# Kernel tuning notes

Measured on AMD Instinct MI355X. Metric: run time of the kernel, lower is better.

The kernel has to match this reference:

```python
import jax, jax.numpy as jnp
import numpy as np
from jax import lax

B, N, F_IN, T = 1024, 22, 32, 32
K = 3
CHEV = 64     # nb_chev_filter
TIMEF = 64    # nb_time_filter
LN_EPS = 1e-5


def setup_inputs() -> dict:
    key = jax.random.key(0)
    ks = jax.random.split(key, 19)
    rn = lambda k, shape, s=0.1: (jax.random.normal(k, shape, jnp.float32) * s)
    return {
        "x": rn(ks[0], (B, N, F_IN, T), 1.0),
        # Temporal_Attention_layer params
        "U1": rn(ks[1], (N,)),
        "U2": rn(ks[2], (F_IN, N)),
        "U3": rn(ks[3], (F_IN,)),
        "be": rn(ks[4], (1, T, T)),
        "Ve": rn(ks[5], (T, T)),
        # Spatial_Attention_layer params
        "W1": rn(ks[6], (T,)),
        "W2": rn(ks[7], (F_IN, T)),
        "W3": rn(ks[8], (F_IN,)),
        "bs": rn(ks[9], (1, N, N)),
        "Vs": rn(ks[10], (N, N)),
        # cheb_conv_withSAt params
        "Theta": rn(ks[11], (K, F_IN, CHEV)),
        "node_emb": rn(ks[12], (N, N), 1.0),
        # time conv (1x3, pad (0,1)) and residual conv (1x1)
        "tconv_w": rn(ks[13], (TIMEF, CHEV, 1, 3)),
        "tconv_b": rn(ks[14], (TIMEF,)),
        "rconv_w": rn(ks[15], (TIMEF, F_IN, 1, 1)),
        "rconv_b": rn(ks[16], (TIMEF,)),
        # LayerNorm over nb_time_filter
        "ln_g": jnp.ones((TIMEF,), jnp.float32),
        "ln_b": jnp.zeros((TIMEF,), jnp.float32),
    }


def reference(x, U1, U2, U3, be, Ve, W1, W2, W3, bs, Vs, Theta, node_emb,
              tconv_w, tconv_b, rconv_w, rconv_b, ln_g, ln_b):
    Bx, Nx, Fx, Tx = x.shape

    # ---- Temporal attention: E_normalized [B, T, T] ----
    # lhs = ((x.permute(0,3,2,1) @ U1) @ U2)  -> [B, T, N]
    lhs_t = jnp.einsum('bnft,n->btf', x, U1) @ U2          # [B,T,N]
    rhs_t = jnp.einsum('f,bnft->bnt', U3, x)               # [B,N,T]
    prod_t = jnp.einsum('btn,bns->bts', lhs_t, rhs_t)      # [B,T,T]
    E = jnp.einsum('ts,bsu->btu', Ve, jax.nn.sigmoid(prod_t + be))
    E_norm = jax.nn.softmax(E, axis=1)                     # softmax over dim=1

    # x_TAt = reshape(x, [B, N*F, T]) @ E_norm  -> [B, N, F, T]
    x_TAt = (x.reshape(Bx, Nx * Fx, Tx) @ E_norm).reshape(Bx, Nx, Fx, Tx)

    # ---- Spatial attention on x_TAt: S_normalized [B, N, N] ----
    lhs_s = jnp.einsum('bnft,t->bnf', x_TAt, W1) @ W2      # [B,N,T]
    rhs_s = jnp.einsum('f,bnft->bnt', W3, x_TAt)           # [B,N,T]
    prod_s = jnp.einsum('bnt,bmt->bnm', lhs_s, rhs_s)      # [B,N,N]
    S = jnp.einsum('nm,bml->bnl', Vs, jax.nn.sigmoid(prod_s + bs))
    S_norm = jax.nn.softmax(S, axis=1)                     # softmax over dim=1

    # ---- Chebyshev graph conv with adaptive supports (vectorized over T) ----
    supports = jax.nn.softmax(jax.nn.relu(node_emb @ node_emb.T), axis=1)
    support_set = [jnp.eye(Nx, dtype=x.dtype), supports]
    for _ in range(2, K):
        support_set.append(2.0 * supports @ support_set[-1] - support_set[-2])

    out = jnp.zeros((Bx, Nx, CHEV, Tx), x.dtype)
    for k in range(K):
        A_k = support_set[k][None, :, :] * S_norm          # [B,N,N]
        # rhs[b,m,f,t] = sum_n A_k[b,n,m] * x[b,n,f,t]  (A_k^T @ graph_signal)
        rhs = jnp.einsum('bnm,bnft->bmft', A_k, x)
        out = out + jnp.einsum('bmft,fo->bmot', rhs, Theta[k])
    spatial_gcn = jax.nn.relu(out)                         # [B,N,CHEV,T]

    # ---- Temporal conv (1x3, pad (0,1)) on [B, CHEV, N, T] ----
    dn = ('NCHW', 'OIHW', 'NCHW')
    t_in = spatial_gcn.transpose(0, 2, 1, 3)               # [B,CHEV,N,T]
    t_out = lax.conv_general_dilated(t_in, tconv_w, (1, 1), ((0, 0), (1, 1)),
                                     dimension_numbers=dn)
    t_out = t_out + tconv_b[None, :, None, None]           # [B,TIMEF,N,T]

    # ---- Residual conv (1x1) on [B, F_in, N, T] ----
    r_in = x.transpose(0, 2, 1, 3)
    r_out = lax.conv_general_dilated(r_in, rconv_w, (1, 1), ((0, 0), (0, 0)),
                                     dimension_numbers=dn)
    r_out = r_out + rconv_b[None, :, None, None]           # [B,TIMEF,N,T]

    # ---- Residual add, ReLU, LayerNorm over channel dim ----
    y = jax.nn.relu(r_out + t_out).transpose(0, 3, 2, 1)   # [B,T,N,TIMEF]
    mu = jnp.mean(y, axis=-1, keepdims=True)
    var = jnp.var(y, axis=-1, keepdims=True)
    y = (y - mu) * lax.rsqrt(var + LN_EPS) * ln_g + ln_b
    return y.transpose(0, 2, 3, 1)                         # [B,N,TIMEF,T]
```

## Files before the change

kernel.cpp:

```cpp
#include <hip/hip_runtime.h>
#include <hip/hip_bf16.h>
#include <math.h>


typedef unsigned short u16;
typedef __attribute__((ext_vector_type(8))) short short8;
typedef __attribute__((ext_vector_type(4))) float f32x4;
typedef __attribute__((ext_vector_type(2))) float f32x2;

__device__ __forceinline__ float sigm(float v){ return 1.f/(1.f+expf(-v)); }

__device__ __forceinline__ u16 f2bf(float x){
  __hip_bfloat16 h = __float2bfloat16(x);
  return *reinterpret_cast<u16*>(&h);
}
__device__ __forceinline__ unsigned f2bf2(float lo, float hi){
  return (unsigned)f2bf(lo) | ((unsigned)f2bf(hi) << 16);
}

__global__ void k_sup_prep(const float* __restrict__ emb, float* __restrict__ wsT,
                           const float* __restrict__ Theta,
                           const float* __restrict__ tw, const float* __restrict__ tb,
                           const float* __restrict__ rw, const float* __restrict__ rb,
                           u16* __restrict__ thA, u16* __restrict__ wA, float* __restrict__ wsB){
  if (blockIdx.x < 81){
    int tid = blockIdx.x*256 + threadIdx.x;
    if (tid < 6144){
      int j = tid&7, l = (tid>>3)&63, blk = tid>>9;
      int ks = blk>>2, ci = blk&3, r = l&15, g = l>>4;
      int kf = 32*ks + 8*g + j, c = 16*ci + r;
      thA[tid] = f2bf(Theta[kf*64 + c]);
    } else if (tid < 20480){
      int e = tid - 6144;
      int j = e&7, l = (e>>3)&63, blk = e>>9;
      int ks = blk>>2, oi = blk&3, r = l&15, g = l>>4;
      int k = 32*ks + 8*g + j, o = 16*oi + r;
      float v = (k < 192) ? tw[o*192 + (k&63)*3 + (k>>6)] : rw[o*32 + (k-192)];
      wA[e] = f2bf(v);
    } else if (tid < 20544){
      int o = tid - 20480; wsB[o] = tb[o] + rb[o];
    }
    return;
  }
  __shared__ float M[484];
  __shared__ float T1s[484];
  int tid = threadIdx.x;
  for (int idx=tid; idx<484; idx+=256){
    int n = idx/22, m = idx - (idx/22)*22;
    float s = 0.f;
    for (int j=0;j<22;j++) s += emb[n*22+j]*emb[m*22+j];
    M[idx] = fmaxf(s, 0.f);
  }
  __syncthreads();
  if (tid < 22){
    float mx = -1e30f;
    for (int m=0;m<22;m++) mx = fmaxf(mx, M[tid*22+m]);
    float s = 0.f;
    for (int m=0;m<22;m++) s += expf(M[tid*22+m]-mx);
    float inv = 1.f/s;
    for (int m=0;m<22;m++) T1s[tid*22+m] = expf(M[tid*22+m]-mx)*inv;
  }
  __syncthreads();
  for (int idx=tid; idx<484; idx+=256){
    int n = idx/22, m = idx - (idx/22)*22;
    float s = 0.f;
    for (int p=0;p<22;p++) s += T1s[n*22+p]*T1s[p*22+m];
    wsT[idx]      = T1s[idx];
    wsT[484+idx]  = 2.f*s - ((n==m)?1.f:0.f);
  }
}

__global__ __launch_bounds__(512) void k_attn(
    const float* __restrict__ x,
    const float* __restrict__ U1, const float* __restrict__ U2, const float* __restrict__ U3,
    const float* __restrict__ be, const float* __restrict__ Ve,
    const float* __restrict__ W1, const float* __restrict__ W2, const float* __restrict__ W3,
    const float* __restrict__ bs, const float* __restrict__ Vs,
    float* __restrict__ snorm){
  int b = blockIdx.x, tid = threadIdx.x;
  const float* xb = x + (size_t)b*22528;
  __shared__ float xu1[1024];
  __shared__ float rhs_t[704];
  __shared__ float lhs_t[704];
  __shared__ float sigp[1024];
  __shared__ float Em[1024];
  __shared__ float sm[1024];
  __shared__ float w1e[32];
  __shared__ float xw3[704];
  __shared__ float lhsS[704];
  __shared__ float lhs2[704];
  __shared__ float rhsS[704];
  __shared__ float sig2[484];
  __shared__ float Sl[484];

  for (int idx=tid; idx<1024; idx+=512){
    float a=0.f;
    for (int n=0;n<22;n++) a = fmaf(xb[n*1024 + idx], U1[n], a);
    xu1[idx]=a;
  }
  for (int idx=tid; idx<704; idx+=512){
    int n = idx>>5, t = idx&31; float a=0.f, c=0.f;
    for (int f=0;f<32;f++){ float xv = xb[n*1024+f*32+t]; a = fmaf(U3[f],xv,a); c = fmaf(W3[f],xv,c); }
    rhs_t[idx]=a; xw3[idx]=c;
  }
  __syncthreads();
  for (int idx=tid; idx<704; idx+=512){
    int t = idx/22, n2 = idx - t*22; float a=0.f;
    for (int f=0;f<32;f++) a = fmaf(xu1[f*32+t], U2[f*22+n2], a);
    lhs_t[idx]=a;
  }
  __syncthreads();
  for (int idx=tid; idx<1024; idx+=512){
    int s = idx>>5, u = idx&31; float p=0.f;
    for (int n=0;n<22;n++) p = fmaf(lhs_t[s*22+n], rhs_t[n*32+u], p);
    sigp[idx] = sigm(p + be[idx]);
  }
  __syncthreads();
  for (int idx=tid; idx<1024; idx+=512){
    int t = idx>>5, u = idx&31; float a=0.f;
    for (int s2=0;s2<32;s2++) a = fmaf(Ve[t*32+s2], sigp[s2*32+u], a);
    Em[idx]=a;
  }
  __syncthreads();
  {
    int u = tid>>4, th = tid&15;
    float e0 = Em[(2*th)*32 + u], e1 = Em[(2*th+1)*32 + u];
    float mx = fmaxf(e0, e1);
    #pragma unroll
    for (int mask=1; mask<16; mask<<=1) mx = fmaxf(mx, __shfl_xor(mx, mask));
    float x0 = expf(e0-mx), x1 = expf(e1-mx);
    float s = x0 + x1;
    #pragma unroll
    for (int mask=1; mask<16; mask<<=1) s += __shfl_xor(s, mask);
    float inv = 1.f/s;
    sm[(2*th)*32 + u]   = x0*inv;
    sm[(2*th+1)*32 + u] = x1*inv;
  }
  __syncthreads();
  {
    int u = tid>>4, th = tid&15;
    float pw = fmaf(sm[u*32 + 2*th], W1[2*th], sm[u*32 + 2*th+1]*W1[2*th+1]);
    #pragma unroll
    for (int mask=1; mask<16; mask<<=1) pw += __shfl_xor(pw, mask);
    if (th==0) w1e[u] = pw;
  }
  __syncthreads();
  for (int idx=tid; idx<704; idx+=512){
    int n = idx>>5, f = idx&31; float a=0.f;
    for (int u=0;u<32;u++) a = fmaf(xb[n*1024+f*32+u], w1e[u], a);
    lhsS[idx]=a;
  }
  __syncthreads();
  for (int idx=tid; idx<704; idx+=512){
    int n = idx>>5, t = idx&31; float a=0.f;
    for (int f=0;f<32;f++) a = fmaf(lhsS[n*32+f], W2[f*32+t], a);
    lhs2[idx]=a;
  }
  for (int idx=tid; idx<704; idx+=512){
    int mm = idx>>5, t = idx&31; float a=0.f;
    for (int u=0;u<32;u++) a = fmaf(xw3[mm*32+u], sm[u*32+t], a);
    rhsS[idx]=a;
  }
  __syncthreads();
  for (int idx=tid; idx<484; idx+=512){
    int a_ = idx/22, l = idx - (idx/22)*22; float p=0.f;
    for (int t=0;t<32;t++) p = fmaf(lhs2[a_*32+t], rhsS[l*32+t], p);
    sig2[idx] = sigm(p + bs[idx]);
  }
  __syncthreads();
  for (int idx=tid; idx<484; idx+=512){
    int n = idx/22, l = idx - (idx/22)*22; float s=0.f;
    for (int mm=0;mm<22;mm++) s = fmaf(Vs[n*22+mm], sig2[mm*22+l], s);
    Sl[idx]=s;
  }
  __syncthreads();
  {
    int grp = tid>>5, nn = tid&31;
    for (int l = grp; l < 22; l += 16){
      float v = (nn<22) ? Sl[nn*22 + l] : -1e30f;
      float mx = v;
      #pragma unroll
      for (int mask=1; mask<32; mask<<=1) mx = fmaxf(mx, __shfl_xor(mx, mask));
      float e = (nn<22) ? expf(v-mx) : 0.f;
      float s = e;
      #pragma unroll
      for (int mask=1; mask<32; mask<<=1) s += __shfl_xor(s, mask);
      if (nn<22) snorm[(size_t)b*484 + nn*22 + l] = e*(1.f/s);
    }
  }
}

__global__ __launch_bounds__(256, 6) void k_fused(
    const float* __restrict__ x,
    const float* __restrict__ wsT, const float* __restrict__ snorm,
    const u16* __restrict__ thA, const u16* __restrict__ wA, const float* __restrict__ wsB,
    const float* __restrict__ lng, const float* __restrict__ lnb,
    float* __restrict__ out){
  __shared__ __align__(16) u16 GtU[2][32*72];
  __shared__ __align__(16) u16 sgTU[2][34*72];
  __shared__ __align__(16) u16 xTU[2][32*40];
  __shared__ __align__(16) float ak4[22*4];
  __shared__ float smm[2];

  int wg = blockIdx.x;
  int logical = (wg & 7)*1408 + (wg >> 3);
  int b = logical/11, mp = logical - b*11;
  int m0 = mp*2;
  int tid = threadIdx.x;
  const float* xb = x + (size_t)b*22528;

  if (tid < 128){
    int mi = tid>>6, r6 = tid&63;
    int row = (r6>>5) ? 33 : 0, c2 = r6&31;
    *(unsigned*)&sgTU[mi][row*72 + c2*2] = 0u;
  }
  if (tid < 88){
    int n = tid>>2, j = tid&3;
    int mi = j>>1, k1 = j&1;
    int m = m0 + mi;
    ak4[tid] = wsT[k1*484 + n*22 + m] * snorm[(size_t)b*484 + n*22 + m];
  }
  if (tid < 2) smm[tid] = snorm[(size_t)b*484 + (m0+tid)*23];
  __syncthreads();

  {
    f32x2 acc[2][2][2];
    #pragma unroll
    for (int a=0;a<2;a++)
      #pragma unroll
      for (int k1=0;k1<2;k1++){ acc[a][k1][0]=f32x2{0,0}; acc[a][k1][1]=f32x2{0,0}; }
    const float4* x4 = (const float4*)xb;
    #pragma unroll 2
    for (int n=0;n<22;n++){
      float4 av = *(const float4*)&ak4[n*4];
      float4 xv = x4[n*256 + tid];
      f32x2 xlo = {xv.x, xv.y}, xhi = {xv.z, xv.w};
      f32x2 a00 = {av.x, av.x}, a01 = {av.y, av.y};
      f32x2 a10 = {av.z, av.z}, a11 = {av.w, av.w};
      acc[0][0][0] = __builtin_elementwise_fma(a00, xlo, acc[0][0][0]);
      acc[0][0][1] = __builtin_elementwise_fma(a00, xhi, acc[0][0][1]);
      acc[0][1][0] = __builtin_elementwise_fma(a01, xlo, acc[0][1][0]);
      acc[0][1][1] = __builtin_elementwise_fma(a01, xhi, acc[0][1][1]);
      acc[1][0][0] = __builtin_elementwise_fma(a10, xlo, acc[1][0][0]);
      acc[1][0][1] = __builtin_elementwise_fma(a10, xhi, acc[1][0][1]);
      acc[1][1][0] = __builtin_elementwise_fma(a11, xlo, acc[1][1][0]);
      acc[1][1][1] = __builtin_elementwise_fma(a11, xhi, acc[1][1][1]);
    }
    int f = tid>>3, t7 = tid&7, t0 = t7*4;
    int w4 = f>>3, f_low = f&7;
    int gcol0 = 8*((0*4 + w4) ^ t7) + f_low;
    int gcol1 = 8*((1*4 + w4) ^ t7) + f_low;
    int xcol  = 8*(w4 ^ (t7&3)) + f_low;
    #pragma unroll
    for (int mi=0;mi<2;mi++){
      float4 xm = ((const float4*)xb)[(m0+mi)*256 + tid];
      u16* xd = &xTU[mi][0];
      xd[(t0+0)*40 + xcol] = f2bf(xm.x);
      xd[(t0+1)*40 + xcol] = f2bf(xm.y);
      xd[(t0+2)*40 + xcol] = f2bf(xm.z);
      xd[(t0+3)*40 + xcol] = f2bf(xm.w);
      #pragma unroll
      for (int k1=0;k1<2;k1++){
        int gc = k1 ? gcol1 : gcol0;
        u16* gd = &GtU[mi][gc];
        gd[(t0+0)*72] = f2bf(acc[mi][k1][0][0]);
        gd[(t0+1)*72] = f2bf(acc[mi][k1][0][1]);
        gd[(t0+2)*72] = f2bf(acc[mi][k1][1][0]);
        gd[(t0+3)*72] = f2bf(acc[mi][k1][1][1]);
      }
    }
  }
  __syncthreads();

  int w = tid>>6, l = tid&63, r = l&15, g = l>>4;

  {
    const u16* tA = thA + (size_t)(w*64 + l)*8;
    short8 a0 = *(const short8*)(tA);
    short8 a1 = *(const short8*)(tA + 2048);
    short8 a2 = *(const short8*)(tA + 4096);
    #pragma unroll
    for (int mi=0;mi<2;mi++){
      float sm_ = smm[mi];
      #pragma unroll
      for (int ti=0; ti<2; ++ti){
        int row = ti*16 + r;
        int h  = (row>>2)&7;
        int h2 = (row>>2)&3;
        f32x4 a12 = {0.f,0.f,0.f,0.f}, ax = {0.f,0.f,0.f,0.f};
        const u16* gp0 = &GtU[mi][row*72 + 8*((0*4+g)^h)];
        const u16* gp1 = &GtU[mi][row*72 + 8*((1*4+g)^h)];
        a12 = __builtin_amdgcn_mfma_f32_16x16x32_bf16(a1, *(const short8*)(gp0), a12, 0,0,0);
        a12 = __builtin_amdgcn_mfma_f32_16x16x32_bf16(a2, *(const short8*)(gp1), a12, 0,0,0);
        const u16* xp = &xTU[mi][row*40 + 8*(g^h2)];
        ax  = __builtin_amdgcn_mfma_f32_16x16x32_bf16(a0, *(const short8*)(xp),  ax,  0,0,0);
        int orow = 1 + row, c0 = w*16 + g*4;
        float v0 = fmaxf(fmaf(sm_, ax[0], a12[0]), 0.f);
        float v1 = fmaxf(fmaf(sm_, ax[1], a12[1]), 0.f);
        float v2 = fmaxf(fmaf(sm_, ax[2], a12[2]), 0.f);
        float v3 = fmaxf(fmaf(sm_, ax[3], a12[3]), 0.f);
        *(unsigned*)&sgTU[mi][orow*72 + c0]     = f2bf2(v0, v1);
        *(unsigned*)&sgTU[mi][orow*72 + c0 + 2] = f2bf2(v2, v3);
      }
    }
  }
  __syncthreads();

  f32x4 acc[2][2];
  acc[0][0]=f32x4{0,0,0,0}; acc[0][1]=f32x4{0,0,0,0};
  acc[1][0]=f32x4{0,0,0,0}; acc[1][1]=f32x4{0,0,0,0};
  {
    const u16* pA = wA + (size_t)(w*64 + l)*8;
    #pragma unroll
    for (int ks=0; ks<6; ++ks){
      short8 wk = *(const short8*)(pA + ks*2048);
      int seg = ks>>1, colb = (ks&1)*32 + 8*g;
      #pragma unroll
      for (int mi=0;mi<2;mi++){
        const u16* q0 = &sgTU[mi][(r + seg)*72 + colb];
        acc[mi][0] = __builtin_amdgcn_mfma_f32_16x16x32_bf16(wk, *(const short8*)(q0),         acc[mi][0], 0,0,0);
        acc[mi][1] = __builtin_amdgcn_mfma_f32_16x16x32_bf16(wk, *(const short8*)(q0 + 16*72), acc[mi][1], 0,0,0);
      }
    }
    short8 wk = *(const short8*)(pA + 6*2048);
    int h2 = (r>>2)&3;
    #pragma unroll
    for (int mi=0;mi<2;mi++){
      const u16* q = &xTU[mi][r*40 + 8*(g^h2)];
      acc[mi][0] = __builtin_amdgcn_mfma_f32_16x16x32_bf16(wk, *(const short8*)(q),         acc[mi][0], 0,0,0);
      acc[mi][1] = __builtin_amdgcn_mfma_f32_16x16x32_bf16(wk, *(const short8*)(q + 16*40), acc[mi][1], 0,0,0);
    }
  }

  float4 bias4 = ((const float4*)wsB)[w*4 + g];
  float bb[4] = {bias4.x, bias4.y, bias4.z, bias4.w};
  float y[2][2][4];
  float s1[2][2] = {{0.f,0.f},{0.f,0.f}}, s2[2][2] = {{0.f,0.f},{0.f,0.f}};
  #pragma unroll
  for (int mi=0;mi<2;mi++){
    #pragma unroll
    for (int h=0;h<2;h++){
      #pragma unroll
      for (int i=0;i<4;i++){
        float v = fmaxf(acc[mi][h][i] + bb[i], 0.f);
        y[mi][h][i] = v;
        s1[mi][h] += v;
        s2[mi][h] = fmaf(v, v, s2[mi][h]);
      }
      s1[mi][h] += __shfl_xor(s1[mi][h],16); s1[mi][h] += __shfl_xor(s1[mi][h],32);
      s2[mi][h] += __shfl_xor(s2[mi][h],16); s2[mi][h] += __shfl_xor(s2[mi][h],32);
    }
  }
  float* p1 = (float*)&GtU[0][0];
  float* p2 = p1 + 256;
  if (l < 16){
    #pragma unroll
    for (int mi=0;mi<2;mi++){
      p1[(mi*32 + l)*4 + w]      = s1[mi][0];
      p1[(mi*32 + 16 + l)*4 + w] = s1[mi][1];
      p2[(mi*32 + l)*4 + w]      = s2[mi][0];
      p2[(mi*32 + 16 + l)*4 + w] = s2[mi][1];
    }
  }
  __syncthreads();
  float4 g4 = ((const float4*)lng)[w*4 + g];
  float4 b4 = ((const float4*)lnb)[w*4 + g];
  float gg[4]={g4.x,g4.y,g4.z,g4.w}, bgg[4]={b4.x,b4.y,b4.z,b4.w};
  #pragma unroll
  for (int mi=0;mi<2;mi++){
    float4 q1a = ((const float4*)p1)[mi*32 + r],      q2a = ((const float4*)p2)[mi*32 + r];
    float4 q1b = ((const float4*)p1)[mi*32 + 16 + r], q2b = ((const float4*)p2)[mi*32 + 16 + r];
    float S1a = q1a.x+q1a.y+q1a.z+q1a.w, S2a = q2a.x+q2a.y+q2a.z+q2a.w;
    float S1b = q1b.x+q1b.y+q1b.z+q1b.w, S2b = q2b.x+q2b.y+q2b.z+q2b.w;
    float mu0 = S1a*(1.f/64.f), var0 = S2a*(1.f/64.f) - mu0*mu0, rs0 = rsqrtf(var0 + 1e-5f);
    float mu1 = S1b*(1.f/64.f), var1 = S2b*(1.f/64.f) - mu1*mu1, rs1 = rsqrtf(var1 + 1e-5f);
    float* ob = out + ((size_t)(b*22 + m0 + mi)*64 + (w*16 + g*4))*32;
    #pragma unroll
    for (int i=0;i<4;i++){
      ob[i*32 + r]      = (y[mi][0][i]-mu0)*rs0*gg[i] + bgg[i];
      ob[i*32 + 16 + r] = (y[mi][1][i]-mu1)*rs1*gg[i] + bgg[i];
    }
  }
}

extern "C" void kernel_launch(void* const* d_in, const int* in_sizes, int n_in,
                              void* d_out, int out_size, void* d_ws, size_t ws_size,
                              hipStream_t stream){
  const float* x     = (const float*)d_in[0];
  const float* U1    = (const float*)d_in[1];
  const float* U2    = (const float*)d_in[2];
  const float* U3    = (const float*)d_in[3];
  const float* be    = (const float*)d_in[4];
  const float* Ve    = (const float*)d_in[5];
  const float* W1    = (const float*)d_in[6];
  const float* W2    = (const float*)d_in[7];
  const float* W3    = (const float*)d_in[8];
  const float* bs    = (const float*)d_in[9];
  const float* Vs    = (const float*)d_in[10];
  const float* Theta = (const float*)d_in[11];
  const float* emb   = (const float*)d_in[12];
  const float* tw    = (const float*)d_in[13];
  const float* tb    = (const float*)d_in[14];
  const float* rw    = (const float*)d_in[15];
  const float* rb    = (const float*)d_in[16];
  const float* lng   = (const float*)d_in[17];
  const float* lnb   = (const float*)d_in[18];
  float* out = (float*)d_out;
  float* wsf = (float*)d_ws;
  float* wsT   = wsf;
  float* snorm = wsf + 1024;
  u16*   thA   = (u16*)(wsf + 496640);
  u16*   wA    = (u16*)(wsf + 499712);
  float* wsB   = wsf + 506880;

  k_sup_prep<<<82, 256, 0, stream>>>(emb, wsT, Theta, tw, tb, rw, rb, thA, wA, wsB);
  k_attn<<<1024, 512, 0, stream>>>(x, U1,U2,U3, be,Ve, W1,W2,W3, bs,Vs, snorm);
  k_fused<<<1024*11, 256, 0, stream>>>(x, wsT, snorm, thA, wA, wsB, lng, lnb, out);
}
```

Baseline: 152.1 us.

## Switch fused kernel MFMAs to 32x32x16 tiles with per-wave node/channel split

Replaces the 16x16x32 bf16 MFMA tiling in both the Chebyshev and temporal-conv GEMMs with 32x32x16 MFMAs. Each wave now owns one output node and one 32-channel half instead of a 16-channel slice across both nodes. Weight pre-packing in the prep kernel is reordered to match. The x gather and the LDS layout are changed to unswizzled, vectorized uint2 stores, and the LayerNorm reduction is simplified to two partial sums. Occupancy bound drops from 6 to 5 to allow the larger accumulators, at the risk of LDS bank conflicts from the removed swizzle.

After: 160.8 us. +5.8%, slower.

```diff
diff --git a/kernel.cpp b/kernel.cpp
--- a/kernel.cpp
+++ b/kernel.cpp
@@ -5,7 +5,7 @@
 
 typedef unsigned short u16;
 typedef __attribute__((ext_vector_type(8))) short short8;
-typedef __attribute__((ext_vector_type(4))) float f32x4;
+typedef __attribute__((ext_vector_type(16))) float f32x16;
 typedef __attribute__((ext_vector_type(2))) float f32x2;
 
 __device__ __forceinline__ float sigm(float v){ return 1.f/(1.f+expf(-v)); }
@@ -26,15 +26,18 @@
   if (blockIdx.x < 81){
     int tid = blockIdx.x*256 + threadIdx.x;
     if (tid < 6144){
-      int j = tid&7, l = (tid>>3)&63, blk = tid>>9;
-      int ks = blk>>2, ci = blk&3, r = l&15, g = l>>4;
-      int kf = 32*ks + 8*g + j, c = 16*ci + r;
-      thA[tid] = f2bf(Theta[kf*64 + c]);
+      int j = tid&7, l = (tid>>3)&63, slot = tid>>9;
+      int fb = slot>>1, ch = slot&1;
+      int hi = l>>5, r = l&31;
+      int row = (fb < 4) ? (32 + 16*fb + 8*hi + j) : (16*(fb-4) + 8*hi + j);
+      thA[tid] = f2bf(Theta[row*64 + 32*ch + r]);
     } else if (tid < 20480){
       int e = tid - 6144;
-      int j = e&7, l = (e>>3)&63, blk = e>>9;
-      int ks = blk>>2, oi = blk&3, r = l&15, g = l>>4;
-      int k = 32*ks + 8*g + j, o = 16*oi + r;
+      int j = e&7, l = (e>>3)&63, slot = e>>9;
+      int kb = slot>>1, oh = slot&1;
+      int hi = l>>5, r = l&31;
+      int k = 16*kb + 8*hi + j;
+      int o = 32*oh + r;
       float v = (k < 192) ? tw[o*192 + (k&63)*3 + (k>>6)] : rw[o*32 + (k-192)];
       wA[e] = f2bf(v);
     } else if (tid < 20544){
@@ -190,7 +193,7 @@
   }
 }
 
-__global__ __launch_bounds__(256, 6) void k_fused(
+__global__ __launch_bounds__(256, 5) void k_fused(
     const float* __restrict__ x,
     const float* __restrict__ wsT, const float* __restrict__ snorm,
     const u16* __restrict__ thA, const u16* __restrict__ wA, const float* __restrict__ wsB,
@@ -210,9 +213,9 @@
   const float* xb = x + (size_t)b*22528;
 
   if (tid < 128){
-    int mi = tid>>6, r6 = tid&63;
-    int row = (r6>>5) ? 33 : 0, c2 = r6&31;
-    *(unsigned*)&sgTU[mi][row*72 + c2*2] = 0u;
+    int mi = tid>>6, c = tid&63;
+    sgTU[mi][c] = 0;
+    sgTU[mi][33*72 + c] = 0;
   }
   if (tid < 88){
     int n = tid>>2, j = tid&3;
@@ -223,162 +226,146 @@
   if (tid < 2) smm[tid] = snorm[(size_t)b*484 + (m0+tid)*23];
   __syncthreads();
 
-  {
-    f32x2 acc[2][2][2];
-    #pragma unroll
-    for (int a=0;a<2;a++)
-      #pragma unroll
-      for (int k1=0;k1<2;k1++){ acc[a][k1][0]=f32x2{0,0}; acc[a][k1][1]=f32x2{0,0}; }
-    const float4* x4 = (const float4*)xb;
+  int t32 = tid&31;
+
+  {
+    int fq = tid>>5, f0 = fq*4;
+    const float* xt = xb + f0*32 + t32;
+    f32x2 acc[4][2];
+    #pragma unroll
+    for (int j=0;j<4;j++){ acc[j][0]=f32x2{0,0}; acc[j][1]=f32x2{0,0}; }
     #pragma unroll 2
     for (int n=0;n<22;n++){
       float4 av = *(const float4*)&ak4[n*4];
-      float4 xv = x4[n*256 + tid];
-      f32x2 xlo = {xv.x, xv.y}, xhi = {xv.z, xv.w};
-      f32x2 a00 = {av.x, av.x}, a01 = {av.y, av.y};
-      f32x2 a10 = {av.z, av.z}, a11 = {av.w, av.w};
-      acc[0][0][0] = __builtin_elementwise_fma(a00, xlo, acc[0][0][0]);
-      acc[0][0][1] = __builtin_elementwise_fma(a00, xhi, acc[0][0][1]);
-      acc[0][1][0] = __builtin_elementwise_fma(a01, xlo, acc[0][1][0]);
-      acc[0][1][1] = __builtin_elementwise_fma(a01, xhi, acc[0][1][1]);
-      acc[1][0][0] = __builtin_elementwise_fma(a10, xlo, acc[1][0][0]);
-      acc[1][0][1] = __builtin_elementwise_fma(a10, xhi, acc[1][0][1]);
-      acc[1][1][0] = __builtin_elementwise_fma(a11, xlo, acc[1][1][0]);
-      acc[1][1][1] = __builtin_elementwise_fma(a11, xhi, acc[1][1][1]);
-    }
-    int f = tid>>3, t7 = tid&7, t0 = t7*4;
-    int w4 = f>>3, f_low = f&7;
-    int gcol0 = 8*((0*4 + w4) ^ t7) + f_low;
-    int gcol1 = 8*((1*4 + w4) ^ t7) + f_low;
-    int xcol  = 8*(w4 ^ (t7&3)) + f_low;
+      const float* p = xt + n*1024;
+      float x0 = p[0], x1 = p[32], x2 = p[64], x3 = p[96];
+      f32x2 lo = {x0,x1}, hi2 = {x2,x3};
+      f32x2 c0 = {av.x,av.x}, c1 = {av.y,av.y}, c2 = {av.z,av.z}, c3 = {av.w,av.w};
+      acc[0][0] = __builtin_elementwise_fma(c0, lo,  acc[0][0]);
+      acc[0][1] = __builtin_elementwise_fma(c0, hi2, acc[0][1]);
+      acc[1][0] = __builtin_elementwise_fma(c1, lo,  acc[1][0]);
+      acc[1][1] = __builtin_elementwise_fma(c1, hi2, acc[1][1]);
+      acc[2][0] = __builtin_elementwise_fma(c2, lo,  acc[2][0]);
+      acc[2][1] = __builtin_elementwise_fma(c2, hi2, acc[2][1]);
+      acc[3][0] = __builtin_elementwise_fma(c3, lo,  acc[3][0]);
+      acc[3][1] = __builtin_elementwise_fma(c3, hi2, acc[3][1]);
+    }
     #pragma unroll
     for (int mi=0;mi<2;mi++){
-      float4 xm = ((const float4*)xb)[(m0+mi)*256 + tid];
-      u16* xd = &xTU[mi][0];
-      xd[(t0+0)*40 + xcol] = f2bf(xm.x);
-      xd[(t0+1)*40 + xcol] = f2bf(xm.y);
-      xd[(t0+2)*40 + xcol] = f2bf(xm.z);
-      xd[(t0+3)*40 + xcol] = f2bf(xm.w);
       #pragma unroll
       for (int k1=0;k1<2;k1++){
-        int gc = k1 ? gcol1 : gcol0;
-        u16* gd = &GtU[mi][gc];
-        gd[(t0+0)*72] = f2bf(acc[mi][k1][0][0]);
-        gd[(t0+1)*72] = f2bf(acc[mi][k1][0][1]);
-        gd[(t0+2)*72] = f2bf(acc[mi][k1][1][0]);
-        gd[(t0+3)*72] = f2bf(acc[mi][k1][1][1]);
+        int j = mi*2 + k1;
+        uint2 v; v.x = f2bf2(acc[j][0][0], acc[j][0][1]); v.y = f2bf2(acc[j][1][0], acc[j][1][1]);
+        *(uint2*)&GtU[mi][t32*72 + k1*32 + f0] = v;
       }
-    }
-  }
-  __syncthreads();
-
-  int w = tid>>6, l = tid&63, r = l&15, g = l>>4;
-
-  {
-    const u16* tA = thA + (size_t)(w*64 + l)*8;
-    short8 a0 = *(const short8*)(tA);
-    short8 a1 = *(const short8*)(tA + 2048);
-    short8 a2 = *(const short8*)(tA + 4096);
-    #pragma unroll
-    for (int mi=0;mi<2;mi++){
-      float sm_ = smm[mi];
+      const float* q = xb + (m0+mi)*1024 + f0*32 + t32;
+      float y0 = q[0], y1 = q[32], y2 = q[64], y3 = q[96];
+      uint2 v; v.x = f2bf2(y0,y1); v.y = f2bf2(y2,y3);
+      *(uint2*)&xTU[mi][t32*40 + f0] = v;
+    }
+  }
+  __syncthreads();
+
+  int w = tid>>6, l = tid&63, hi = l>>5;
+  int mi = w>>1, ch = w&1;
+  int lt = l&31;
+
+  {
+    f32x16 aG, aX;
+    #pragma unroll
+    for (int i=0;i<16;i++){ aG[i]=0.f; aX[i]=0.f; }
+    const u16* gRow = &GtU[mi][lt*72 + 8*hi];
+    const u16* xRow = &xTU[mi][lt*40 + 8*hi];
+    #pragma unroll
+    for (int fb=0; fb<4; ++fb){
+      short8 a = *(const short8*)(thA + (size_t)(fb*2+ch)*512 + l*8);
+      aG = __builtin_amdgcn_mfma_f32_32x32x16_bf16(a, *(const short8*)(gRow + 16*fb), aG, 0,0,0);
+    }
+    #pragma unroll
+    for (int fb=4; fb<6; ++fb){
+      short8 a = *(const short8*)(thA + (size_t)(fb*2+ch)*512 + l*8);
+      aX = __builtin_amdgcn_mfma_f32_32x32x16_bf16(a, *(const short8*)(xRow + 16*(fb-4)), aX, 0,0,0);
+    }
+    float smv = smm[mi];
+    u16* srow = &sgTU[mi][(1+lt)*72 + ch*32 + 4*hi];
+    #pragma unroll
+    for (int q=0;q<4;q++){
+      float v0 = fmaxf(fmaf(smv, aX[4*q+0], aG[4*q+0]), 0.f);
+      float v1 = fmaxf(fmaf(smv, aX[4*q+1], aG[4*q+1]), 0.f);
+      float v2 = fmaxf(fmaf(smv, aX[4*q+2], aG[4*q+2]), 0.f);
+      float v3 = fmaxf(fmaf(smv, aX[4*q+3], aG[4*q+3]), 0.f);
+      uint2 pv; pv.x = f2bf2(v0,v1); pv.y = f2bf2(v2,v3);
+      *(uint2*)&srow[8*q] = pv;
+    }
+  }
+  __syncthreads();
+
+  f32x16 acc;
+  #pragma unroll
+  for (int i=0;i<16;i++) acc[i]=0.f;
+  {
+    #pragma unroll
+    for (int kb=0; kb<12; ++kb){
+      int dt = kb>>2, cq = kb&3;
+      short8 wk = *(const short8*)(wA + (size_t)(kb*2+ch)*512 + l*8);
+      const short8* Bp = (const short8*)&sgTU[mi][(lt+dt)*72 + cq*16 + 8*hi];
+      acc = __builtin_amdgcn_mfma_f32_32x32x16_bf16(wk, *Bp, acc, 0,0,0);
+    }
+    #pragma unroll
+    for (int kb=12; kb<14; ++kb){
+      short8 wk = *(const short8*)(wA + (size_t)(kb*2+ch)*512 + l*8);
+      const short8* Bp = (const short8*)&xTU[mi][lt*40 + (kb-12)*16 + 8*hi];
+      acc = __builtin_amdgcn_mfma_f32_32x32x16_bf16(wk, *Bp, acc, 0,0,0);
+    }
+  }
+
+  float y[16];
+  float s1 = 0.f, s2 = 0.f;
+  {
+    const float4* wsB4 = (const float4*)wsB;
+    #pragma unroll
+    for (int q=0;q<4;q++){
+      float4 bq = wsB4[8*ch + 2*q + hi];
+      float bb[4] = {bq.x, bq.y, bq.z, bq.w};
       #pragma unroll
-      for (int ti=0; ti<2; ++ti){
-        int row = ti*16 + r;
-        int h  = (row>>2)&7;
-        int h2 = (row>>2)&3;
-        f32x4 a12 = {0.f,0.f,0.f,0.f}, ax = {0.f,0.f,0.f,0.f};
-        const u16* gp0 = &GtU[mi][row*72 + 8*((0*4+g)^h)];
-        const u16* gp1 = &GtU[mi][row*72 + 8*((1*4+g)^h)];
-        a12 = __builtin_amdgcn_mfma_f32_16x16x32_bf16(a1, *(const short8*)(gp0), a12, 0,0,0);
-        a12 = __builtin_amdgcn_mfma_f32_16x16x32_bf16(a2, *(const short8*)(gp1), a12, 0,0,0);
-        const u16* xp = &xTU[mi][row*40 + 8*(g^h2)];
-        ax  = __builtin_amdgcn_mfma_f32_16x16x32_bf16(a0, *(const short8*)(xp),  ax,  0,0,0);
-        int orow = 1 + row, c0 = w*16 + g*4;
-        float v0 = fmaxf(fmaf(sm_, ax[0], a12[0]), 0.f);
-        float v1 = fmaxf(fmaf(sm_, ax[1], a12[1]), 0.f);
-        float v2 = fmaxf(fmaf(sm_, ax[2], a12[2]), 0.f);
-        float v3 = fmaxf(fmaf(sm_, ax[3], a12[3]), 0.f);
-        *(unsigned*)&sgTU[mi][orow*72 + c0]     = f2bf2(v0, v1);
-        *(unsigned*)&sgTU[mi][orow*72 + c0 + 2] = f2bf2(v2, v3);
+      for (int e=0;e<4;e++){
+        float v = fmaxf(acc[4*q+e] + bb[e], 0.f);
+        y[4*q+e] = v;
+        s1 += v;
+        s2 = fmaf(v, v, s2);
       }
     }
   }
-  __syncthreads();
-
-  f32x4 acc[2][2];
-  acc[0][0]=f32x4{0,0,0,0}; acc[0][1]=f32x4{0,0,0,0};
-  acc[1][0]=f32x4{0,0,0,0}; acc[1][1]=f32x4{0,0,0,0};
-  {
-    const u16* pA = wA + (size_t)(w*64 + l)*8;
-    #pragma unroll
-    for (int ks=0; ks<6; ++ks){
-      short8 wk = *(const short8*)(pA + ks*2048);
-      int seg = ks>>1, colb = (ks&1)*32 + 8*g;
+  s1 += __shfl_xor(s1, 32);
+  s2 += __shfl_xor(s2, 32);
+  float* p1 = (float*)&GtU[0][0];
+  float* p2 = p1 + 128;
+  if (l < 32){
+    p1[(mi*32 + lt)*2 + ch] = s1;
+    p2[(mi*32 + lt)*2 + ch] = s2;
+  }
+  __syncthreads();
+  f32x2 q1 = *(const f32x2*)&p1[(mi*32 + lt)*2];
+  f32x2 q2 = *(const f32x2*)&p2[(mi*32 + lt)*2];
+  float S1 = q1[0] + q1[1], S2 = q2[0] + q2[1];
+  float mu = S1*(1.f/64.f);
+  float var = S2*(1.f/64.f) - mu*mu;
+  float rs = rsqrtf(var + 1e-5f);
+  {
+    const float4* lng4 = (const float4*)lng;
+    const float4* lnb4 = (const float4*)lnb;
+    float* ob = out + ((size_t)(b*22 + m0 + mi)*64 + 32*ch)*32;
+    #pragma unroll
+    for (int q=0;q<4;q++){
+      float4 g4 = lng4[8*ch + 2*q + hi];
+      float4 b4 = lnb4[8*ch + 2*q + hi];
+      float gg[4] = {g4.x,g4.y,g4.z,g4.w};
+      float bg[4] = {b4.x,b4.y,b4.z,b4.w};
       #pragma unroll
-      for (int mi=0;mi<2;mi++){
-        const u16* q0 = &sgTU[mi][(r + seg)*72 + colb];
-        acc[mi][0] = __builtin_amdgcn_mfma_f32_16x16x32_bf16(wk, *(const short8*)(q0),         acc[mi][0], 0,0,0);
-        acc[mi][1] = __builtin_amdgcn_mfma_f32_16x16x32_bf16(wk, *(const short8*)(q0 + 16*72), acc[mi][1], 0,0,0);
+      for (int e=0;e<4;e++){
+        int orow = 8*q + 4*hi + e;
+        ob[orow*32 + lt] = (y[4*q+e]-mu)*rs*gg[e] + bg[e];
       }
-    }
-    short8 wk = *(const short8*)(pA + 6*2048);
-    int h2 = (r>>2)&3;
-    #pragma unroll
-    for (int mi=0;mi<2;mi++){
-      const u16* q = &xTU[mi][r*40 + 8*(g^h2)];
-      acc[mi][0] = __builtin_amdgcn_mfma_f32_16x16x32_bf16(wk, *(const short8*)(q),         acc[mi][0], 0,0,0);
-      acc[mi][1] = __builtin_amdgcn_mfma_f32_16x16x32_bf16(wk, *(const short8*)(q + 16*40), acc[mi][1], 0,0,0);
-    }
-  }
-
-  float4 bias4 = ((const float4*)wsB)[w*4 + g];
-  float bb[4] = {bias4.x, bias4.y, bias4.z, bias4.w};
-  float y[2][2][4];
-  float s1[2][2] = {{0.f,0.f},{0.f,0.f}}, s2[2][2] = {{0.f,0.f},{0.f,0.f}};
-  #pragma unroll
-  for (int mi=0;mi<2;mi++){
-    #pragma unroll
-    for (int h=0;h<2;h++){
-      #pragma unroll
-      for (int i=0;i<4;i++){
-        float v = fmaxf(acc[mi][h][i] + bb[i], 0.f);
-        y[mi][h][i] = v;
-        s1[mi][h] += v;
-        s2[mi][h] = fmaf(v, v, s2[mi][h]);
-      }
-      s1[mi][h] += __shfl_xor(s1[mi][h],16); s1[mi][h] += __shfl_xor(s1[mi][h],32);
-      s2[mi][h] += __shfl_xor(s2[mi][h],16); s2[mi][h] += __shfl_xor(s2[mi][h],32);
-    }
-  }
-  float* p1 = (float*)&GtU[0][0];
-  float* p2 = p1 + 256;
-  if (l < 16){
-    #pragma unroll
-    for (int mi=0;mi<2;mi++){
-      p1[(mi*32 + l)*4 + w]      = s1[mi][0];
-      p1[(mi*32 + 16 + l)*4 + w] = s1[mi][1];
-      p2[(mi*32 + l)*4 + w]      = s2[mi][0];
-      p2[(mi*32 + 16 + l)*4 + w] = s2[mi][1];
-    }
-  }
-  __syncthreads();
-  float4 g4 = ((const float4*)lng)[w*4 + g];
-  float4 b4 = ((const float4*)lnb)[w*4 + g];
-  float gg[4]={g4.x,g4.y,g4.z,g4.w}, bgg[4]={b4.x,b4.y,b4.z,b4.w};
-  #pragma unroll
-  for (int mi=0;mi<2;mi++){
-    float4 q1a = ((const float4*)p1)[mi*32 + r],      q2a = ((const float4*)p2)[mi*32 + r];
-    float4 q1b = ((const float4*)p1)[mi*32 + 16 + r], q2b = ((const float4*)p2)[mi*32 + 16 + r];
-    float S1a = q1a.x+q1a.y+q1a.z+q1a.w, S2a = q2a.x+q2a.y+q2a.z+q2a.w;
-    float S1b = q1b.x+q1b.y+q1b.z+q1b.w, S2b = q2b.x+q2b.y+q2b.z+q2b.w;
-    float mu0 = S1a*(1.f/64.f), var0 = S2a*(1.f/64.f) - mu0*mu0, rs0 = rsqrtf(var0 + 1e-5f);
-    float mu1 = S1b*(1.f/64.f), var1 = S2b*(1.f/64.f) - mu1*mu1, rs1 = rsqrtf(var1 + 1e-5f);
-    float* ob = out + ((size_t)(b*22 + m0 + mi)*64 + (w*16 + g*4))*32;
-    #pragma unroll
-    for (int i=0;i<4;i++){
-      ob[i*32 + r]      = (y[mi][0][i]-mu0)*rs0*gg[i] + bgg[i];
-      ob[i*32 + 16 + r] = (y[mi][1][i]-mu1)*rs1*gg[i] + bgg[i];
     }
   }
 }
```

## Split attention kernel in two and fold weight prep into the first

Applied to the files above, without the earlier changes.

Splits the monolithic attention kernel into two kernels. The first computes the temporal-attention softmax, w1e and xw3 and writes them to global workspace. The second reloads them and computes spatial attention, so each kernel holds less shared memory and can run more blocks per CU. The separate setup kernel (weight packing, Chebyshev supports) is merged into extra blocks of the first kernel to save a launch. The lhsS dot product is vectorised with float4 loads. The cost is an extra global round trip of roughly 7 MB of intermediates plus another kernel boundary.

Result: no change. 153.9 us (+1.2%).

```diff
diff --git a/kernel.cpp b/kernel.cpp
--- a/kernel.cpp
+++ b/kernel.cpp
@@ -18,136 +18,170 @@
   return (unsigned)f2bf(lo) | ((unsigned)f2bf(hi) << 16);
 }
 
-__global__ void k_sup_prep(const float* __restrict__ emb, float* __restrict__ wsT,
-                           const float* __restrict__ Theta,
-                           const float* __restrict__ tw, const float* __restrict__ tb,
-                           const float* __restrict__ rw, const float* __restrict__ rb,
-                           u16* __restrict__ thA, u16* __restrict__ wA, float* __restrict__ wsB){
-  if (blockIdx.x < 81){
-    int tid = blockIdx.x*256 + threadIdx.x;
-    if (tid < 6144){
-      int j = tid&7, l = (tid>>3)&63, blk = tid>>9;
-      int ks = blk>>2, ci = blk&3, r = l&15, g = l>>4;
-      int kf = 32*ks + 8*g + j, c = 16*ci + r;
-      thA[tid] = f2bf(Theta[kf*64 + c]);
-    } else if (tid < 20480){
-      int e = tid - 6144;
-      int j = e&7, l = (e>>3)&63, blk = e>>9;
-      int ks = blk>>2, oi = blk&3, r = l&15, g = l>>4;
-      int k = 32*ks + 8*g + j, o = 16*oi + r;
-      float v = (k < 192) ? tw[o*192 + (k&63)*3 + (k>>6)] : rw[o*32 + (k-192)];
-      wA[e] = f2bf(v);
-    } else if (tid < 20544){
-      int o = tid - 20480; wsB[o] = tb[o] + rb[o];
-    }
-    return;
-  }
-  __shared__ float M[484];
-  __shared__ float T1s[484];
-  int tid = threadIdx.x;
-  for (int idx=tid; idx<484; idx+=256){
-    int n = idx/22, m = idx - (idx/22)*22;
-    float s = 0.f;
-    for (int j=0;j<22;j++) s += emb[n*22+j]*emb[m*22+j];
-    M[idx] = fmaxf(s, 0.f);
-  }
-  __syncthreads();
-  if (tid < 22){
-    float mx = -1e30f;
-    for (int m=0;m<22;m++) mx = fmaxf(mx, M[tid*22+m]);
-    float s = 0.f;
-    for (int m=0;m<22;m++) s += expf(M[tid*22+m]-mx);
-    float inv = 1.f/s;
-    for (int m=0;m<22;m++) T1s[tid*22+m] = expf(M[tid*22+m]-mx)*inv;
-  }
-  __syncthreads();
-  for (int idx=tid; idx<484; idx+=256){
-    int n = idx/22, m = idx - (idx/22)*22;
-    float s = 0.f;
-    for (int p=0;p<22;p++) s += T1s[n*22+p]*T1s[p*22+m];
-    wsT[idx]      = T1s[idx];
-    wsT[484+idx]  = 2.f*s - ((n==m)?1.f:0.f);
-  }
-}
-
-__global__ __launch_bounds__(512) void k_attn(
+__global__ __launch_bounds__(512) void k_attnA(
     const float* __restrict__ x,
     const float* __restrict__ U1, const float* __restrict__ U2, const float* __restrict__ U3,
-    const float* __restrict__ be, const float* __restrict__ Ve,
-    const float* __restrict__ W1, const float* __restrict__ W2, const float* __restrict__ W3,
-    const float* __restrict__ bs, const float* __restrict__ Vs,
-    float* __restrict__ snorm){
-  int b = blockIdx.x, tid = threadIdx.x;
-  const float* xb = x + (size_t)b*22528;
+    const float* __restrict__ be, const float* __restrict__ Ve, const float* __restrict__ W1,
+    const float* __restrict__ W3,
+    float* __restrict__ smG, float* __restrict__ w1eG, float* __restrict__ xw3G,
+    const float* __restrict__ emb, float* __restrict__ wsT,
+    const float* __restrict__ Theta,
+    const float* __restrict__ tw, const float* __restrict__ tb,
+    const float* __restrict__ rw, const float* __restrict__ rb,
+    u16* __restrict__ thA, u16* __restrict__ wA, float* __restrict__ wsB){
   __shared__ float xu1[1024];
   __shared__ float rhs_t[704];
   __shared__ float lhs_t[704];
   __shared__ float sigp[1024];
   __shared__ float Em[1024];
   __shared__ float sm[1024];
+  __shared__ float xw3[704];
   __shared__ float w1e[32];
+
+  int bid = blockIdx.x, tid = threadIdx.x;
+
+  if (bid >= 1024){
+    int pb = bid - 1024;
+    if (pb < 41){
+      int t2 = pb*512 + tid;
+      if (t2 < 6144){
+        int j = t2&7, l = (t2>>3)&63, blk = t2>>9;
+        int ks = blk>>2, ci = blk&3, r = l&15, g = l>>4;
+        int kf = 32*ks + 8*g + j, c = 16*ci + r;
+        thA[t2] = f2bf(Theta[kf*64 + c]);
+      } else if (t2 < 20480){
+        int e = t2 - 6144;
+        int j = e&7, l = (e>>3)&63, blk = e>>9;
+        int ks = blk>>2, oi = blk&3, r = l&15, g = l>>4;
+        int k = 32*ks + 8*g + j, o = 16*oi + r;
+        float v = (k < 192) ? tw[o*192 + (k&63)*3 + (k>>6)] : rw[o*32 + (k-192)];
+        wA[e] = f2bf(v);
+      } else if (t2 < 20544){
+        int o = t2 - 20480; wsB[o] = tb[o] + rb[o];
+      }
+      return;
+    }
+    float* M   = &xu1[0];
+    float* T1s = &sigp[0];
+    for (int idx=tid; idx<484; idx+=512){
+      int n = idx/22, m = idx - (idx/22)*22;
+      float s = 0.f;
+      for (int j=0;j<22;j++) s += emb[n*22+j]*emb[m*22+j];
+      M[idx] = fmaxf(s, 0.f);
+    }
+    __syncthreads();
+    if (tid < 22){
+      float mx = -1e30f;
+      for (int m=0;m<22;m++) mx = fmaxf(mx, M[tid*22+m]);
+      float s = 0.f;
+      for (int m=0;m<22;m++) s += expf(M[tid*22+m]-mx);
+      float inv = 1.f/s;
+      for (int m=0;m<22;m++) T1s[tid*22+m] = expf(M[tid*22+m]-mx)*inv;
+    }
+    __syncthreads();
+    for (int idx=tid; idx<484; idx+=512){
+      int n = idx/22, m = idx - (idx/22)*22;
+      float s = 0.f;
+      for (int p=0;p<22;p++) s += T1s[n*22+p]*T1s[p*22+m];
+      wsT[idx]      = T1s[idx];
+      wsT[484+idx]  = 2.f*s - ((n==m)?1.f:0.f);
+    }
+    return;
+  }
+
+  int b = bid;
+  const float* xb = x + (size_t)b*22528;
+
+  for (int idx=tid; idx<1024; idx+=512){
+    float a=0.f;
+    for (int n=0;n<22;n++) a = fmaf(xb[n*1024 + idx], U1[n], a);
+    xu1[idx]=a;
+  }
+  for (int idx=tid; idx<704; idx+=512){
+    int n = idx>>5, t = idx&31; float a=0.f, c=0.f;
+    for (int f=0;f<32;f++){ float xv = xb[n*1024+f*32+t]; a = fmaf(U3[f],xv,a); c = fmaf(W3[f],xv,c); }
+    rhs_t[idx]=a; xw3[idx]=c;
+  }
+  __syncthreads();
+  for (int idx=tid; idx<704; idx+=512){
+    int t = idx/22, n2 = idx - t*22; float a=0.f;
+    for (int f=0;f<32;f++) a = fmaf(xu1[f*32+t], U2[f*22+n2], a);
+    lhs_t[idx]=a;
+  }
+  __syncthreads();
+  for (int idx=tid; idx<1024; idx+=512){
+    int s = idx>>5, u = idx&31; float p=0.f;
+    for (int n=0;n<22;n++) p = fmaf(lhs_t[s*22+n], rhs_t[n*32+u], p);
+    sigp[idx] = sigm(p + be[idx]);
+  }
+  __syncthreads();
+  for (int idx=tid; idx<1024; idx+=512){
+    int t = idx>>5, u = idx&31; float a=0.f;
+    for (int s2=0;s2<32;s2++) a = fmaf(Ve[t*32+s2], sigp[s2*32+u], a);
+    Em[idx]=a;
+  }
+  __syncthreads();
+  {
+    int u = tid>>4, th = tid&15;
+    float e0 = Em[(2*th)*32 + u], e1 = Em[(2*th+1)*32 + u];
+    float mx = fmaxf(e0, e1);
+    #pragma unroll
+    for (int mask=1; mask<16; mask<<=1) mx = fmaxf(mx, __shfl_xor(mx, mask));
+    float x0 = expf(e0-mx), x1 = expf(e1-mx);
+    float s = x0 + x1;
+    #pragma unroll
+    for (int mask=1; mask<16; mask<<=1) s += __shfl_xor(s, mask);
+    float inv = 1.f/s;
+    sm[(2*th)*32 + u]   = x0*inv;
+    sm[(2*th+1)*32 + u] = x1*inv;
+  }
+  __syncthreads();
+  {
+    int u = tid>>4, th = tid&15;
+    float pw = fmaf(sm[u*32 + 2*th], W1[2*th], sm[u*32 + 2*th+1]*W1[2*th+1]);
+    #pragma unroll
+    for (int mask=1; mask<16; mask<<=1) pw += __shfl_xor(pw, mask);
+    if (th==0) w1e[u] = pw;
+  }
+  __syncthreads();
+  for (int idx=tid; idx<1024; idx+=512) smG[(size_t)b*1024 + idx] = sm[idx];
+  for (int idx=tid; idx<704; idx+=512)  xw3G[(size_t)b*704 + idx] = xw3[idx];
+  if (tid < 32) w1eG[b*32 + tid] = w1e[tid];
+}
+
+__global__ __launch_bounds__(512) void k_attnB(
+    const float* __restrict__ x,
+    const float* __restrict__ W2, const float* __restrict__ bs, const float* __restrict__ Vs,
+    const float* __restrict__ smG, const float* __restrict__ w1eG, const float* __restrict__ xw3G,
+    float* __restrict__ snorm){
+  __shared__ float sm[1024];
   __shared__ float xw3[704];
+  __shared__ float w1e[32];
   __shared__ float lhsS[704];
   __shared__ float lhs2[704];
   __shared__ float rhsS[704];
   __shared__ float sig2[484];
   __shared__ float Sl[484];
 
-  for (int idx=tid; idx<1024; idx+=512){
-    float a=0.f;
-    for (int n=0;n<22;n++) a = fmaf(xb[n*1024 + idx], U1[n], a);
-    xu1[idx]=a;
-  }
+  int b = blockIdx.x, tid = threadIdx.x;
+  const float* xb = x + (size_t)b*22528;
+
+  for (int idx=tid; idx<1024; idx+=512) sm[idx] = smG[(size_t)b*1024 + idx];
+  for (int idx=tid; idx<704; idx+=512)  xw3[idx] = xw3G[(size_t)b*704 + idx];
+  if (tid < 32) w1e[tid] = w1eG[b*32 + tid];
+  __syncthreads();
+
   for (int idx=tid; idx<704; idx+=512){
-    int n = idx>>5, t = idx&31; float a=0.f, c=0.f;
-    for (int f=0;f<32;f++){ float xv = xb[n*1024+f*32+t]; a = fmaf(U3[f],xv,a); c = fmaf(W3[f],xv,c); }
-    rhs_t[idx]=a; xw3[idx]=c;
-  }
-  __syncthreads();
-  for (int idx=tid; idx<704; idx+=512){
-    int t = idx/22, n2 = idx - t*22; float a=0.f;
-    for (int f=0;f<32;f++) a = fmaf(xu1[f*32+t], U2[f*22+n2], a);
-    lhs_t[idx]=a;
-  }
-  __syncthreads();
-  for (int idx=tid; idx<1024; idx+=512){
-    int s = idx>>5, u = idx&31; float p=0.f;
-    for (int n=0;n<22;n++) p = fmaf(lhs_t[s*22+n], rhs_t[n*32+u], p);
-    sigp[idx] = sigm(p + be[idx]);
-  }
-  __syncthreads();
-  for (int idx=tid; idx<1024; idx+=512){
-    int t = idx>>5, u = idx&31; float a=0.f;
-    for (int s2=0;s2<32;s2++) a = fmaf(Ve[t*32+s2], sigp[s2*32+u], a);
-    Em[idx]=a;
-  }
-  __syncthreads();
-  {
-    int u = tid>>4, th = tid&15;
-    float e0 = Em[(2*th)*32 + u], e1 = Em[(2*th+1)*32 + u];
-    float mx = fmaxf(e0, e1);
-    #pragma unroll
-    for (int mask=1; mask<16; mask<<=1) mx = fmaxf(mx, __shfl_xor(mx, mask));
-    float x0 = expf(e0-mx), x1 = expf(e1-mx);
-    float s = x0 + x1;
-    #pragma unroll
-    for (int mask=1; mask<16; mask<<=1) s += __shfl_xor(s, mask);
-    float inv = 1.f/s;
-    sm[(2*th)*32 + u]   = x0*inv;
-    sm[(2*th+1)*32 + u] = x1*inv;
-  }
-  __syncthreads();
-  {
-    int u = tid>>4, th = tid&15;
-    float pw = fmaf(sm[u*32 + 2*th], W1[2*th], sm[u*32 + 2*th+1]*W1[2*th+1]);
-    #pragma unroll
-    for (int mask=1; mask<16; mask<<=1) pw += __shfl_xor(pw, mask);
-    if (th==0) w1e[u] = pw;
-  }
-  __syncthreads();
-  for (int idx=tid; idx<704; idx+=512){
-    int n = idx>>5, f = idx&31; float a=0.f;
-    for (int u=0;u<32;u++) a = fmaf(xb[n*1024+f*32+u], w1e[u], a);
+    int n = idx>>5, f = idx&31;
+    const float4* xp = (const float4*)(xb + n*1024 + f*32);
+    const float4* wv = (const float4*)w1e;
+    float a = 0.f;
+    #pragma unroll
+    for (int q=0;q<8;q++){
+      float4 xv = xp[q], w4 = wv[q];
+      a = fmaf(xv.x, w4.x, a); a = fmaf(xv.y, w4.y, a);
+      a = fmaf(xv.z, w4.z, a); a = fmaf(xv.w, w4.w, a);
+    }
     lhsS[idx]=a;
   }
   __syncthreads();
@@ -224,27 +258,24 @@
   __syncthreads();
 
   {
-    f32x2 acc[2][2][2];
-    #pragma unroll
-    for (int a=0;a<2;a++)
-      #pragma unroll
-      for (int k1=0;k1<2;k1++){ acc[a][k1][0]=f32x2{0,0}; acc[a][k1][1]=f32x2{0,0}; }
+    f32x2 acc[4][2];
+    #pragma unroll
+    for (int j=0;j<4;j++){ acc[j][0]=f32x2{0,0}; acc[j][1]=f32x2{0,0}; }
     const float4* x4 = (const float4*)xb;
     #pragma unroll 2
     for (int n=0;n<22;n++){
       float4 av = *(const float4*)&ak4[n*4];
       float4 xv = x4[n*256 + tid];
-      f32x2 xlo = {xv.x, xv.y}, xhi = {xv.z, xv.w};
-      f32x2 a00 = {av.x, av.x}, a01 = {av.y, av.y};
-      f32x2 a10 = {av.z, av.z}, a11 = {av.w, av.w};
-      acc[0][0][0] = __builtin_elementwise_fma(a00, xlo, acc[0][0][0]);
-      acc[0][0][1] = __builtin_elementwise_fma(a00, xhi, acc[0][0][1]);
-      acc[0][1][0] = __builtin_elementwise_fma(a01, xlo, acc[0][1][0]);
-      acc[0][1][1] = __builtin_elementwise_fma(a01, xhi, acc[0][1][1]);
-      acc[1][0][0] = __builtin_elementwise_fma(a10, xlo, acc[1][0][0]);
-      acc[1][0][1] = __builtin_elementwise_fma(a10, xhi, acc[1][0][1]);
-      acc[1][1][0] = __builtin_elementwise_fma(a11, xlo, acc[1][1][0]);
-      acc[1][1][1] = __builtin_elementwise_fma(a11, xhi, acc[1][1][1]);
+      f32x2 xlo = {xv.x, xv.y}, xhi2 = {xv.z, xv.w};
+      f32x2 c0 = {av.x,av.x}, c1 = {av.y,av.y}, c2 = {av.z,av.z}, c3 = {av.w,av.w};
+      acc[0][0] = __builtin_elementwise_fma(c0, xlo,  acc[0][0]);
+      acc[0][1] = __builtin_elementwise_fma(c0, xhi2, acc[0][1]);
+      acc[1][0] = __builtin_elementwise_fma(c1, xlo,  acc[1][0]);
+      acc[1][1] = __builtin_elementwise_fma(c1, xhi2, acc[1][1]);
+      acc[2][0] = __builtin_elementwise_fma(c2, xlo,  acc[2][0]);
+      acc[2][1] = __builtin_elementwise_fma(c2, xhi2, acc[2][1]);
+      acc[3][0] = __builtin_elementwise_fma(c3, xlo,  acc[3][0]);
+      acc[3][1] = __builtin_elementwise_fma(c3, xhi2, acc[3][1]);
     }
     int f = tid>>3, t7 = tid&7, t0 = t7*4;
     int w4 = f>>3, f_low = f&7;
@@ -261,12 +292,13 @@
       xd[(t0+3)*40 + xcol] = f2bf(xm.w);
       #pragma unroll
       for (int k1=0;k1<2;k1++){
+        int j = mi*2 + k1;
         int gc = k1 ? gcol1 : gcol0;
         u16* gd = &GtU[mi][gc];
-        gd[(t0+0)*72] = f2bf(acc[mi][k1][0][0]);
-        gd[(t0+1)*72] = f2bf(acc[mi][k1][0][1]);
-        gd[(t0+2)*72] = f2bf(acc[mi][k1][1][0]);
-        gd[(t0+3)*72] = f2bf(acc[mi][k1][1][1]);
+        gd[(t0+0)*72] = f2bf(acc[j][0][0]);
+        gd[(t0+1)*72] = f2bf(acc[j][0][1]);
+        gd[(t0+2)*72] = f2bf(acc[j][1][0]);
+        gd[(t0+3)*72] = f2bf(acc[j][1][1]);
       }
     }
   }
@@ -412,8 +444,12 @@
   u16*   thA   = (u16*)(wsf + 496640);
   u16*   wA    = (u16*)(wsf + 499712);
   float* wsB   = wsf + 506880;
-
-  k_sup_prep<<<82, 256, 0, stream>>>(emb, wsT, Theta, tw, tb, rw, rb, thA, wA, wsB);
-  k_attn<<<1024, 512, 0, stream>>>(x, U1,U2,U3, be,Ve, W1,W2,W3, bs,Vs, snorm);
+  float* smG   = wsf + 507904;
+  float* xw3G  = wsf + 1556480;
+  float* w1eG  = wsf + 2277376;
+
+  k_attnA<<<1066, 512, 0, stream>>>(x, U1,U2,U3, be,Ve, W1, W3, smG, w1eG, xw3G,
+                                    emb, wsT, Theta, tw, tb, rw, rb, thA, wA, wsB);
+  k_attnB<<<1024, 512, 0, stream>>>(x, W2, bs, Vs, smG, w1eG, xw3G, snorm);
   k_fused<<<1024*11, 256, 0, stream>>>(x, wsT, snorm, thA, wA, wsB, lng, lnb, out);
 }
```
